# Optimization experiments

Hardware: AMD Instinct MI355X
Metric: run time of the kernel (lower is better)

Reference implementation:

```python
import jax, jax.numpy as jnp
import numpy as np

B, S, D = 16, 2048, 128

def setup_inputs() -> dict:
    key = jax.random.key(0)
    kq, kk, kv = jax.random.split(key, 3)
    queries = jax.random.normal(kq, (B, S, D), dtype=jnp.float32)
    keys = jax.random.normal(kk, (B, S, D), dtype=jnp.float32)
    values = jax.random.normal(kv, (B, S, D), dtype=jnp.float32)
    return {"queries": queries, "keys": keys, "values": values}

def reference(queries, keys, values):
    # scores: [B, S, S] = Q @ K^T / sqrt(D)
    d = queries.shape[-1]
    scores = jnp.einsum('bqd,bkd->bqk', queries, keys) / jnp.float32(np.sqrt(d))
    attn = jax.nn.softmax(scores, axis=-1)
    # dropout_rate=0.0 -> identity
    out = jnp.einsum('bqk,bkd->bqd', attn, values)
    return out
```

## Files before the change

kernel.cpp:

```cpp
#include <hip/hip_runtime.h>
#include <hip/hip_bf16.h>

#define BATCH 16
#define SEQ   2048
#define DIM   128
#define KTILE 64
#define NIT   (SEQ / KTILE)
#define NITP  (NIT / 2)
#define QT    128
#define SCALE2 (0.08838834764831845f * 1.4426950408889634f)

typedef __bf16 bf16_t;
typedef __bf16 bf16x8 __attribute__((ext_vector_type(8)));
typedef __bf16 bf16x4 __attribute__((ext_vector_type(4)));
typedef float  f32x4  __attribute__((ext_vector_type(4)));

#define KSTR 136

__device__ __forceinline__ int rho(int s) {
    return (s & 32) | ((s & 4) << 2) | (((s >> 3) & 3) << 2) | (s & 3);
}
__device__ __forceinline__ int swz(int row) {
    return (row & 7) ^ ((row >> 2) & 7);
}

__global__ __launch_bounds__(512, 2)
void attn_fwd(const float* __restrict__ Qg, const float* __restrict__ Kg,
              const float* __restrict__ Vg, float* __restrict__ Og)
{
    __shared__ __align__(16) bf16_t sK [4][KTILE][KSTR];
    __shared__ __align__(16) bf16_t sVt[4][DIM][64];

    const int tid  = threadIdx.x;
    const int wave = tid >> 6;
    const int lane = tid & 63;
    const int l16  = lane & 15;
    const int g    = lane >> 4;
    const bool is_comp = (wave < 4);

    const int bid   = blockIdx.x;
    const int batch = ((bid & 7) << 1) | ((bid >> 7) & 1);
    const int qtile = (bid >> 3) & 15;
    const int q0    = qtile * QT + wave * 32;

    const float* Kb = Kg + (size_t)batch * SEQ * DIM;
    const float* Vb = Vg + (size_t)batch * SEQ * DIM;

    bf16x8 qf[2][4];
    if (is_comp) {
        #pragma unroll
        for (int h = 0; h < 2; ++h) {
            const float* qp =
                Qg + ((size_t)batch * SEQ + q0 + h * 16 + l16) * DIM + g * 8;
            #pragma unroll
            for (int c = 0; c < 4; ++c) {
                const float4 u = *reinterpret_cast<const float4*>(qp + c * 32);
                const float4 v = *reinterpret_cast<const float4*>(qp + c * 32 + 4);
                bf16x8 f;
                f[0] = (bf16_t)(u.x * SCALE2); f[1] = (bf16_t)(u.y * SCALE2);
                f[2] = (bf16_t)(u.z * SCALE2); f[3] = (bf16_t)(u.w * SCALE2);
                f[4] = (bf16_t)(v.x * SCALE2); f[5] = (bf16_t)(v.y * SCALE2);
                f[6] = (bf16_t)(v.z * SCALE2); f[7] = (bf16_t)(v.w * SCALE2);
                qf[h][c] = f;
            }
        }
    }

    const int p    = tid & 255;
    const int krow = p >> 3;
    const int kch  = p & 7;
    const int vkg  = p >> 5;
    const int vd4  = p & 31;

    auto stage = [&](int k0, int buf) {
        float4 ka[2][2][2];
        float4 va[2][4];
        #pragma unroll
        for (int r = 0; r < 2; ++r)
            #pragma unroll
            for (int i = 0; i < 2; ++i) {
                const float* pp =
                    Kb + (size_t)(k0 + krow + r * 32) * DIM + kch * 8 + i * 64;
                ka[r][i][0] = *reinterpret_cast<const float4*>(pp);
                ka[r][i][1] = *reinterpret_cast<const float4*>(pp + 4);
            }
        #pragma unroll
        for (int r = 0; r < 2; ++r)
            #pragma unroll
            for (int j = 0; j < 4; ++j)
                va[r][j] = *reinterpret_cast<const float4*>(
                    Vb + (size_t)(k0 + (vkg + r * 8) * 4 + j) * DIM + vd4 * 4);
        #pragma unroll
        for (int r = 0; r < 2; ++r) {
            const int row = krow + r * 32;
            #pragma unroll
            for (int i = 0; i < 2; ++i) {
                const float* a = reinterpret_cast<const float*>(&ka[r][i][0]);
                bf16x8 w;
                #pragma unroll
                for (int e = 0; e < 8; ++e) w[e] = (bf16_t)a[e];
                *reinterpret_cast<bf16x8*>(&sK[buf][rho(row)][kch * 8 + i * 64]) = w;
            }
            const int kg = vkg + r * 8;
            #pragma unroll
            for (int dd = 0; dd < 4; ++dd) {
                const int vrow = vd4 * 4 + dd;
                const int col = (((kg >> 1) ^ swz(vrow)) << 3) + ((kg & 1) << 2);
                bf16x4 w;
                w[0] = (bf16_t)va[r][0][dd]; w[1] = (bf16_t)va[r][1][dd];
                w[2] = (bf16_t)va[r][2][dd]; w[3] = (bf16_t)va[r][3][dd];
                *reinterpret_cast<bf16x4*>(&sVt[buf][vrow][col]) = w;
            }
        }
    };

    const f32x4 vzero = {0.f, 0.f, 0.f, 0.f};
    f32x4 o[2][8];
    float lsum[2];
    if (is_comp) {
        #pragma unroll
        for (int h = 0; h < 2; ++h) {
            #pragma unroll
            for (int i = 0; i < 8; ++i) o[h][i] = vzero;
            lsum[h] = 0.f;
        }
    }

    if (!is_comp) {
        stage(0, 0);
        __builtin_amdgcn_sched_barrier(0);
        stage(KTILE, 1);
    }

    for (int t = 0; t < NITP; ++t) {
        __syncthreads();

        if (!is_comp) {
            if (t + 1 < NITP) {
                stage((2 * t + 2) * KTILE, (2 * t + 2) & 3);
                __builtin_amdgcn_sched_barrier(0);
                stage((2 * t + 3) * KTILE, (2 * t + 3) & 3);
            }
            continue;
        }

        #pragma unroll
        for (int s = 0; s < 2; ++s) {
            const int cur = (2 * t + s) & 3;

            f32x4 sc[2][4];
            #pragma unroll
            for (int ksb = 0; ksb < 4; ++ksb) { sc[0][ksb] = vzero; sc[1][ksb] = vzero; }
            __builtin_amdgcn_s_setprio(1);
            #pragma unroll
            for (int c = 0; c < 4; ++c) {
                #pragma unroll
                for (int ksb = 0; ksb < 4; ++ksb) {
                    bf16x8 kf = *reinterpret_cast<const bf16x8*>(
                        &sK[cur][ksb * 16 + l16][c * 32 + g * 8]);
                    sc[0][ksb] = __builtin_amdgcn_mfma_f32_16x16x32_bf16(
                        kf, qf[0][c], sc[0][ksb], 0, 0, 0);
                    sc[1][ksb] = __builtin_amdgcn_mfma_f32_16x16x32_bf16(
                        kf, qf[1][c], sc[1][ksb], 0, 0, 0);
                }
            }
            __builtin_amdgcn_s_setprio(0);

            float pe[2][16];
            #pragma unroll
            for (int h = 0; h < 2; ++h)
                #pragma unroll
                for (int ksb = 0; ksb < 4; ++ksb)
                    #pragma unroll
                    for (int r = 0; r < 4; ++r)
                        pe[h][ksb * 4 + r] = exp2f(sc[h][ksb][r]);
            #pragma unroll
            for (int h = 0; h < 2; ++h) {
                const float s0 = (pe[h][0] + pe[h][1]) + (pe[h][2] + pe[h][3]);
                const float s1 = (pe[h][4] + pe[h][5]) + (pe[h][6] + pe[h][7]);
                const float s2 = (pe[h][8] + pe[h][9]) + (pe[h][10] + pe[h][11]);
                const float s3 = (pe[h][12] + pe[h][13]) + (pe[h][14] + pe[h][15]);
                lsum[h] += (s0 + s1) + (s2 + s3);
            }
            bf16x8 pb[2][2];
            #pragma unroll
            for (int h = 0; h < 2; ++h)
                #pragma unroll
                for (int c2 = 0; c2 < 2; ++c2) {
                    bf16x8 tt;
                    #pragma unroll
                    for (int jj = 0; jj < 8; ++jj)
                        tt[jj] = (bf16_t)pe[h][(2 * c2 + (jj >> 2)) * 4 + (jj & 3)];
                    pb[h][c2] = tt;
                }

            __builtin_amdgcn_s_setprio(1);
            #pragma unroll
            for (int n0 = 0; n0 < 8; ++n0) {
                const int row = n0 * 16 + l16;
                #pragma unroll
                for (int c2 = 0; c2 < 2; ++c2) {
                    bf16x8 vf = *reinterpret_cast<const bf16x8*>(
                        &sVt[cur][row][((c2 * 4 + g) ^ swz(row)) << 3]);
                    o[0][n0] = __builtin_amdgcn_mfma_f32_16x16x32_bf16(
                        vf, pb[0][c2], o[0][n0], 0, 0, 0);
                    o[1][n0] = __builtin_amdgcn_mfma_f32_16x16x32_bf16(
                        vf, pb[1][c2], o[1][n0], 0, 0, 0);
                }
            }
            __builtin_amdgcn_s_setprio(0);
        }
    }

    if (is_comp) {
        #pragma unroll
        for (int h = 0; h < 2; ++h) {
            float l = lsum[h];
            l += __shfl_xor(l, 16);
            l += __shfl_xor(l, 32);
            const float inv = 1.f / l;
            float* op = Og + ((size_t)batch * SEQ + q0 + h * 16 + l16) * DIM + g * 4;
            #pragma unroll
            for (int n0 = 0; n0 < 8; ++n0) {
                float4 st = { o[h][n0][0] * inv, o[h][n0][1] * inv,
                              o[h][n0][2] * inv, o[h][n0][3] * inv };
                *reinterpret_cast<float4*>(op + n0 * 16) = st;
            }
        }
    }
}

extern "C" void kernel_launch(void* const* d_in, const int* in_sizes, int n_in,
                              void* d_out, int out_size, void* d_ws, size_t ws_size,
                              hipStream_t stream) {
    const float* Q = (const float*)d_in[0];
    const float* K = (const float*)d_in[1];
    const float* V = (const float*)d_in[2];
    float* O = (float*)d_out;
    dim3 grid(BATCH * SEQ / QT);
    dim3 block(512);
    hipLaunchKernelGGL(attn_fwd, grid, block, 0, stream, Q, K, V, O);
}
```

Before: 127.9 us.

## Split KV sequence across block pairs with cooperative grid sync to combine

```diff
diff --git a/kernel.cpp b/kernel.cpp
--- a/kernel.cpp
+++ b/kernel.cpp
@@ -1,13 +1,16 @@
 #include <hip/hip_runtime.h>
 #include <hip/hip_bf16.h>
+#include <hip/hip_cooperative_groups.h>
+
+namespace cg = cooperative_groups;
 
 #define BATCH 16
 #define SEQ   2048
 #define DIM   128
 #define KTILE 64
-#define NIT   (SEQ / KTILE)
-#define NITP  (NIT / 2)
-#define QT    128
+#define HALF  (SEQ / 2)
+#define NB    (HALF / KTILE)
+#define QT    256
 #define SCALE2 (0.08838834764831845f * 1.4426950408889634f)
 
 typedef __bf16 bf16_t;
@@ -26,204 +29,208 @@
 
 __global__ __launch_bounds__(512, 2)
 void attn_fwd(const float* __restrict__ Qg, const float* __restrict__ Kg,
-              const float* __restrict__ Vg, float* __restrict__ Og)
+              const float* __restrict__ Vg, float* __restrict__ Og,
+              float* __restrict__ lws)
 {
-    __shared__ __align__(16) bf16_t sK [4][KTILE][KSTR];
-    __shared__ __align__(16) bf16_t sVt[4][DIM][64];
+    __shared__ __align__(16) bf16_t sK [2][KTILE][KSTR];
+    __shared__ __align__(16) bf16_t sVt[2][DIM][64];
 
     const int tid  = threadIdx.x;
     const int wave = tid >> 6;
     const int lane = tid & 63;
     const int l16  = lane & 15;
     const int g    = lane >> 4;
-    const bool is_comp = (wave < 4);
 
     const int bid   = blockIdx.x;
-    const int batch = ((bid & 7) << 1) | ((bid >> 7) & 1);
-    const int qtile = (bid >> 3) & 15;
-    const int q0    = qtile * QT + wave * 32;
-
-    const float* Kb = Kg + (size_t)batch * SEQ * DIM;
-    const float* Vb = Vg + (size_t)batch * SEQ * DIM;
+    const int qt    = bid >> 1;
+    const int kv    = bid & 1;
+    const int batch = qt >> 3;
+    const int q0    = (qt & 7) * QT + wave * 32;
+
+    const float* Kb = Kg + ((size_t)batch * SEQ + kv * HALF) * DIM;
+    const float* Vb = Vg + ((size_t)batch * SEQ + kv * HALF) * DIM;
 
     bf16x8 qf[2][4];
-    if (is_comp) {
-        #pragma unroll
-        for (int h = 0; h < 2; ++h) {
-            const float* qp =
-                Qg + ((size_t)batch * SEQ + q0 + h * 16 + l16) * DIM + g * 8;
-            #pragma unroll
-            for (int c = 0; c < 4; ++c) {
-                const float4 u = *reinterpret_cast<const float4*>(qp + c * 32);
-                const float4 v = *reinterpret_cast<const float4*>(qp + c * 32 + 4);
-                bf16x8 f;
-                f[0] = (bf16_t)(u.x * SCALE2); f[1] = (bf16_t)(u.y * SCALE2);
-                f[2] = (bf16_t)(u.z * SCALE2); f[3] = (bf16_t)(u.w * SCALE2);
-                f[4] = (bf16_t)(v.x * SCALE2); f[5] = (bf16_t)(v.y * SCALE2);
-                f[6] = (bf16_t)(v.z * SCALE2); f[7] = (bf16_t)(v.w * SCALE2);
-                qf[h][c] = f;
-            }
-        }
-    }
-
-    const int p    = tid & 255;
-    const int krow = p >> 3;
-    const int kch  = p & 7;
-    const int vkg  = p >> 5;
-    const int vd4  = p & 31;
-
-    auto stage = [&](int k0, int buf) {
-        float4 ka[2][2][2];
-        float4 va[2][4];
-        #pragma unroll
-        for (int r = 0; r < 2; ++r)
-            #pragma unroll
-            for (int i = 0; i < 2; ++i) {
-                const float* pp =
-                    Kb + (size_t)(k0 + krow + r * 32) * DIM + kch * 8 + i * 64;
-                ka[r][i][0] = *reinterpret_cast<const float4*>(pp);
-                ka[r][i][1] = *reinterpret_cast<const float4*>(pp + 4);
-            }
-        #pragma unroll
-        for (int r = 0; r < 2; ++r)
-            #pragma unroll
-            for (int j = 0; j < 4; ++j)
-                va[r][j] = *reinterpret_cast<const float4*>(
-                    Vb + (size_t)(k0 + (vkg + r * 8) * 4 + j) * DIM + vd4 * 4);
-        #pragma unroll
-        for (int r = 0; r < 2; ++r) {
-            const int row = krow + r * 32;
-            #pragma unroll
-            for (int i = 0; i < 2; ++i) {
-                const float* a = reinterpret_cast<const float*>(&ka[r][i][0]);
-                bf16x8 w;
-                #pragma unroll
-                for (int e = 0; e < 8; ++e) w[e] = (bf16_t)a[e];
-                *reinterpret_cast<bf16x8*>(&sK[buf][rho(row)][kch * 8 + i * 64]) = w;
-            }
-            const int kg = vkg + r * 8;
-            #pragma unroll
-            for (int dd = 0; dd < 4; ++dd) {
-                const int vrow = vd4 * 4 + dd;
-                const int col = (((kg >> 1) ^ swz(vrow)) << 3) + ((kg & 1) << 2);
-                bf16x4 w;
-                w[0] = (bf16_t)va[r][0][dd]; w[1] = (bf16_t)va[r][1][dd];
-                w[2] = (bf16_t)va[r][2][dd]; w[3] = (bf16_t)va[r][3][dd];
-                *reinterpret_cast<bf16x4*>(&sVt[buf][vrow][col]) = w;
-            }
+    #pragma unroll
+    for (int h = 0; h < 2; ++h) {
+        const float* qp =
+            Qg + ((size_t)batch * SEQ + q0 + h * 16 + l16) * DIM + g * 8;
+        #pragma unroll
+        for (int c = 0; c < 4; ++c) {
+            const float4 u = *reinterpret_cast<const float4*>(qp + c * 32);
+            const float4 v = *reinterpret_cast<const float4*>(qp + c * 32 + 4);
+            bf16x8 f;
+            f[0] = (bf16_t)(u.x * SCALE2); f[1] = (bf16_t)(u.y * SCALE2);
+            f[2] = (bf16_t)(u.z * SCALE2); f[3] = (bf16_t)(u.w * SCALE2);
+            f[4] = (bf16_t)(v.x * SCALE2); f[5] = (bf16_t)(v.y * SCALE2);
+            f[6] = (bf16_t)(v.z * SCALE2); f[7] = (bf16_t)(v.w * SCALE2);
+            qf[h][c] = f;
+        }
+    }
+
+    const int krow = tid >> 3;
+    const int kch  = tid & 7;
+    const int vkg  = tid >> 5;
+    const int vd4  = tid & 31;
+
+    float4 gka[2][2];
+    float4 gva[4];
+
+    auto load_tile = [&](int k0) {
+        #pragma unroll
+        for (int i = 0; i < 2; ++i) {
+            const float* pp = Kb + (size_t)(k0 + krow) * DIM + kch * 8 + i * 64;
+            gka[i][0] = *reinterpret_cast<const float4*>(pp);
+            gka[i][1] = *reinterpret_cast<const float4*>(pp + 4);
+        }
+        #pragma unroll
+        for (int j = 0; j < 4; ++j)
+            gva[j] = *reinterpret_cast<const float4*>(
+                Vb + (size_t)(k0 + vkg * 4 + j) * DIM + vd4 * 4);
+    };
+    auto write_tile = [&](int buf) {
+        #pragma unroll
+        for (int i = 0; i < 2; ++i) {
+            const float* a = reinterpret_cast<const float*>(&gka[i][0]);
+            bf16x8 w;
+            #pragma unroll
+            for (int e = 0; e < 8; ++e) w[e] = (bf16_t)a[e];
+            *reinterpret_cast<bf16x8*>(&sK[buf][rho(krow)][kch * 8 + i * 64]) = w;
+        }
+        #pragma unroll
+        for (int dd = 0; dd < 4; ++dd) {
+            const int row = vd4 * 4 + dd;
+            const int col = (((vkg >> 1) ^ swz(row)) << 3) + ((vkg & 1) << 2);
+            bf16x4 w;
+            w[0] = (bf16_t)gva[0][dd]; w[1] = (bf16_t)gva[1][dd];
+            w[2] = (bf16_t)gva[2][dd]; w[3] = (bf16_t)gva[3][dd];
+            *reinterpret_cast<bf16x4*>(&sVt[buf][row][col]) = w;
         }
     };
 
     const f32x4 vzero = {0.f, 0.f, 0.f, 0.f};
     f32x4 o[2][8];
     float lsum[2];
-    if (is_comp) {
+    #pragma unroll
+    for (int h = 0; h < 2; ++h) {
+        #pragma unroll
+        for (int i = 0; i < 8; ++i) o[h][i] = vzero;
+        lsum[h] = 0.f;
+    }
+
+    load_tile(0);
+    write_tile(0);
+    load_tile(KTILE);
+    __syncthreads();
+
+    for (int t = 0; t < NB; ++t) {
+        const int cur = t & 1;
+
+        f32x4 sc[2][4];
+        #pragma unroll
+        for (int ksb = 0; ksb < 4; ++ksb) { sc[0][ksb] = vzero; sc[1][ksb] = vzero; }
+        __builtin_amdgcn_s_setprio(1);
+        #pragma unroll
+        for (int c = 0; c < 4; ++c) {
+            #pragma unroll
+            for (int ksb = 0; ksb < 4; ++ksb) {
+                bf16x8 kf = *reinterpret_cast<const bf16x8*>(
+                    &sK[cur][ksb * 16 + l16][c * 32 + g * 8]);
+                sc[0][ksb] = __builtin_amdgcn_mfma_f32_16x16x32_bf16(
+                    kf, qf[0][c], sc[0][ksb], 0, 0, 0);
+                sc[1][ksb] = __builtin_amdgcn_mfma_f32_16x16x32_bf16(
+                    kf, qf[1][c], sc[1][ksb], 0, 0, 0);
+            }
+        }
+        __builtin_amdgcn_s_setprio(0);
+
+        if (t + 1 < NB) write_tile(cur ^ 1);
+        if (t + 2 < NB) load_tile((t + 2) * KTILE);
+
+        float pe[2][16];
+        #pragma unroll
+        for (int h = 0; h < 2; ++h)
+            #pragma unroll
+            for (int ksb = 0; ksb < 4; ++ksb)
+                #pragma unroll
+                for (int r = 0; r < 4; ++r)
+                    pe[h][ksb * 4 + r] = exp2f(sc[h][ksb][r]);
         #pragma unroll
         for (int h = 0; h < 2; ++h) {
-            #pragma unroll
-            for (int i = 0; i < 8; ++i) o[h][i] = vzero;
-            lsum[h] = 0.f;
-        }
-    }
-
-    if (!is_comp) {
-        stage(0, 0);
-        __builtin_amdgcn_sched_barrier(0);
-        stage(KTILE, 1);
-    }
-
-    for (int t = 0; t < NITP; ++t) {
+            const float s0 = (pe[h][0] + pe[h][1]) + (pe[h][2] + pe[h][3]);
+            const float s1 = (pe[h][4] + pe[h][5]) + (pe[h][6] + pe[h][7]);
+            const float s2 = (pe[h][8] + pe[h][9]) + (pe[h][10] + pe[h][11]);
+            const float s3 = (pe[h][12] + pe[h][13]) + (pe[h][14] + pe[h][15]);
+            lsum[h] += (s0 + s1) + (s2 + s3);
+        }
+        bf16x8 pb[2][2];
+        #pragma unroll
+        for (int h = 0; h < 2; ++h)
+            #pragma unroll
+            for (int c2 = 0; c2 < 2; ++c2) {
+                bf16x8 tt;
+                #pragma unroll
+                for (int jj = 0; jj < 8; ++jj)
+                    tt[jj] = (bf16_t)pe[h][(2 * c2 + (jj >> 2)) * 4 + (jj & 3)];
+                pb[h][c2] = tt;
+            }
+
+        __builtin_amdgcn_s_setprio(1);
+        #pragma unroll
+        for (int n0 = 0; n0 < 8; ++n0) {
+            const int row = n0 * 16 + l16;
+            #pragma unroll
+            for (int c2 = 0; c2 < 2; ++c2) {
+                bf16x8 vf = *reinterpret_cast<const bf16x8*>(
+                    &sVt[cur][row][((c2 * 4 + g) ^ swz(row)) << 3]);
+                o[0][n0] = __builtin_amdgcn_mfma_f32_16x16x32_bf16(
+                    vf, pb[0][c2], o[0][n0], 0, 0, 0);
+                o[1][n0] = __builtin_amdgcn_mfma_f32_16x16x32_bf16(
+                    vf, pb[1][c2], o[1][n0], 0, 0, 0);
+            }
+        }
+        __builtin_amdgcn_s_setprio(0);
+
         __syncthreads();
-
-        if (!is_comp) {
-            if (t + 1 < NITP) {
-                stage((2 * t + 2) * KTILE, (2 * t + 2) & 3);
-                __builtin_amdgcn_sched_barrier(0);
-                stage((2 * t + 3) * KTILE, (2 * t + 3) & 3);
-            }
-            continue;
-        }
-
-        #pragma unroll
-        for (int s = 0; s < 2; ++s) {
-            const int cur = (2 * t + s) & 3;
-
-            f32x4 sc[2][4];
-            #pragma unroll
-            for (int ksb = 0; ksb < 4; ++ksb) { sc[0][ksb] = vzero; sc[1][ksb] = vzero; }
-            __builtin_amdgcn_s_setprio(1);
-            #pragma unroll
-            for (int c = 0; c < 4; ++c) {
-                #pragma unroll
-                for (int ksb = 0; ksb < 4; ++ksb) {
-                    bf16x8 kf = *reinterpret_cast<const bf16x8*>(
-                        &sK[cur][ksb * 16 + l16][c * 32 + g * 8]);
-                    sc[0][ksb] = __builtin_amdgcn_mfma_f32_16x16x32_bf16(
-                        kf, qf[0][c], sc[0][ksb], 0, 0, 0);
-                    sc[1][ksb] = __builtin_amdgcn_mfma_f32_16x16x32_bf16(
-                        kf, qf[1][c], sc[1][ksb], 0, 0, 0);
-                }
-            }
-            __builtin_amdgcn_s_setprio(0);
-
-            float pe[2][16];
-            #pragma unroll
-            for (int h = 0; h < 2; ++h)
-                #pragma unroll
-                for (int ksb = 0; ksb < 4; ++ksb)
-                    #pragma unroll
-                    for (int r = 0; r < 4; ++r)
-                        pe[h][ksb * 4 + r] = exp2f(sc[h][ksb][r]);
-            #pragma unroll
-            for (int h = 0; h < 2; ++h) {
-                const float s0 = (pe[h][0] + pe[h][1]) + (pe[h][2] + pe[h][3]);
-                const float s1 = (pe[h][4] + pe[h][5]) + (pe[h][6] + pe[h][7]);
-                const float s2 = (pe[h][8] + pe[h][9]) + (pe[h][10] + pe[h][11]);
-                const float s3 = (pe[h][12] + pe[h][13]) + (pe[h][14] + pe[h][15]);
-                lsum[h] += (s0 + s1) + (s2 + s3);
-            }
-            bf16x8 pb[2][2];
-            #pragma unroll
-            for (int h = 0; h < 2; ++h)
-                #pragma unroll
-                for (int c2 = 0; c2 < 2; ++c2) {
-                    bf16x8 tt;
-                    #pragma unroll
-                    for (int jj = 0; jj < 8; ++jj)
-                        tt[jj] = (bf16_t)pe[h][(2 * c2 + (jj >> 2)) * 4 + (jj & 3)];
-                    pb[h][c2] = tt;
-                }
-
-            __builtin_amdgcn_s_setprio(1);
+    }
+
+    float l[2];
+    #pragma unroll
+    for (int h = 0; h < 2; ++h) {
+        float v = lsum[h];
+        v += __shfl_xor(v, 16);
+        v += __shfl_xor(v, 32);
+        l[h] = v;
+    }
+
+    if (kv == 0) {
+        #pragma unroll
+        for (int h = 0; h < 2; ++h) {
+            float* op = Og + ((size_t)batch * SEQ + q0 + h * 16 + l16) * DIM + g * 4;
             #pragma unroll
             for (int n0 = 0; n0 < 8; ++n0) {
-                const int row = n0 * 16 + l16;
-                #pragma unroll
-                for (int c2 = 0; c2 < 2; ++c2) {
-                    bf16x8 vf = *reinterpret_cast<const bf16x8*>(
-                        &sVt[cur][row][((c2 * 4 + g) ^ swz(row)) << 3]);
-                    o[0][n0] = __builtin_amdgcn_mfma_f32_16x16x32_bf16(
-                        vf, pb[0][c2], o[0][n0], 0, 0, 0);
-                    o[1][n0] = __builtin_amdgcn_mfma_f32_16x16x32_bf16(
-                        vf, pb[1][c2], o[1][n0], 0, 0, 0);
-                }
-            }
-            __builtin_amdgcn_s_setprio(0);
-        }
-    }
-
-    if (is_comp) {
+                float4 st = { o[h][n0][0], o[h][n0][1], o[h][n0][2], o[h][n0][3] };
+                *reinterpret_cast<float4*>(op + n0 * 16) = st;
+            }
+            if (g == 0) lws[qt * QT + wave * 32 + h * 16 + l16] = l[h];
+        }
+    }
+    __threadfence();
+    cg::this_grid().sync();
+    __threadfence();
+    if (kv == 1) {
         #pragma unroll
         for (int h = 0; h < 2; ++h) {
-            float l = lsum[h];
-            l += __shfl_xor(l, 16);
-            l += __shfl_xor(l, 32);
-            const float inv = 1.f / l;
+            const float l0 = lws[qt * QT + wave * 32 + h * 16 + l16];
+            const float inv = 1.f / (l0 + l[h]);
             float* op = Og + ((size_t)batch * SEQ + q0 + h * 16 + l16) * DIM + g * 4;
             #pragma unroll
             for (int n0 = 0; n0 < 8; ++n0) {
-                float4 st = { o[h][n0][0] * inv, o[h][n0][1] * inv,
-                              o[h][n0][2] * inv, o[h][n0][3] * inv };
+                const float4 pr = *reinterpret_cast<const float4*>(op + n0 * 16);
+                float4 st = { (o[h][n0][0] + pr.x) * inv,
+                              (o[h][n0][1] + pr.y) * inv,
+                              (o[h][n0][2] + pr.z) * inv,
+                              (o[h][n0][3] + pr.w) * inv };
                 *reinterpret_cast<float4*>(op + n0 * 16) = st;
             }
         }
@@ -237,7 +244,9 @@
     const float* K = (const float*)d_in[1];
     const float* V = (const float*)d_in[2];
     float* O = (float*)d_out;
-    dim3 grid(BATCH * SEQ / QT);
+    float* lws = (float*)d_ws;
+    void* args[] = { (void*)&Q, (void*)&K, (void*)&V, (void*)&O, (void*)&lws };
+    dim3 grid(BATCH * SEQ / QT * 2);
     dim3 block(512);
-    hipLaunchKernelGGL(attn_fwd, grid, block, 0, stream, Q, K, V, O);
-}
+    hipLaunchCooperativeKernel((void*)attn_fwd, grid, block, args, 0, stream);
+}
```

New measurement: 278.6 us. +117.8%, slower.

## Split KV sequence across blocks with partial outputs and combine kernel

Applied to the files above, without the earlier changes.

```diff
diff --git a/kernel.cpp b/kernel.cpp
--- a/kernel.cpp
+++ b/kernel.cpp
@@ -5,9 +5,10 @@
 #define SEQ   2048
 #define DIM   128
 #define KTILE 64
-#define NIT   (SEQ / KTILE)
-#define NITP  (NIT / 2)
-#define QT    128
+#define HALF  (SEQ / 2)
+#define NB    (HALF / KTILE)
+#define QT    256
+#define NROW  (BATCH * SEQ)
 #define SCALE2 (0.08838834764831845f * 1.4426950408889634f)
 
 typedef __bf16 bf16_t;
@@ -25,8 +26,221 @@
 }
 
 __global__ __launch_bounds__(512, 2)
-void attn_fwd(const float* __restrict__ Qg, const float* __restrict__ Kg,
-              const float* __restrict__ Vg, float* __restrict__ Og)
+void attn_fwd_partial(const float* __restrict__ Qg, const float* __restrict__ Kg,
+                      const float* __restrict__ Vg, float* __restrict__ Og,
+                      float* __restrict__ lws)
+{
+    __shared__ __align__(16) bf16_t sK [2][KTILE][KSTR];
+    __shared__ __align__(16) bf16_t sVt[2][DIM][64];
+
+    const int tid  = threadIdx.x;
+    const int wave = tid >> 6;
+    const int lane = tid & 63;
+    const int l16  = lane & 15;
+    const int g    = lane >> 4;
+
+    const int bid  = blockIdx.x;
+    const int xcd  = bid & 7;
+    const int idx  = bid >> 3;
+    const int qtl  = idx & 7;
+    const int rest = idx >> 3;
+    const int sb   = rest & 1;
+    const int kv   = rest >> 1;
+    const int batch = (xcd << 1) | sb;
+    const int q0    = qtl * QT + wave * 32;
+
+    const float* Kb = Kg + ((size_t)batch * SEQ + kv * HALF) * DIM;
+    const float* Vb = Vg + ((size_t)batch * SEQ + kv * HALF) * DIM;
+
+    bf16x8 qf[2][4];
+    #pragma unroll
+    for (int h = 0; h < 2; ++h) {
+        const float* qp =
+            Qg + ((size_t)batch * SEQ + q0 + h * 16 + l16) * DIM + g * 8;
+        #pragma unroll
+        for (int c = 0; c < 4; ++c) {
+            const float4 u = *reinterpret_cast<const float4*>(qp + c * 32);
+            const float4 v = *reinterpret_cast<const float4*>(qp + c * 32 + 4);
+            bf16x8 f;
+            f[0] = (bf16_t)(u.x * SCALE2); f[1] = (bf16_t)(u.y * SCALE2);
+            f[2] = (bf16_t)(u.z * SCALE2); f[3] = (bf16_t)(u.w * SCALE2);
+            f[4] = (bf16_t)(v.x * SCALE2); f[5] = (bf16_t)(v.y * SCALE2);
+            f[6] = (bf16_t)(v.z * SCALE2); f[7] = (bf16_t)(v.w * SCALE2);
+            qf[h][c] = f;
+        }
+    }
+
+    const int krow = tid >> 3;
+    const int kch  = tid & 7;
+    const int vkg  = tid >> 5;
+    const int vd4  = tid & 31;
+
+    float4 gka[2][2];
+    float4 gva[4];
+
+    auto load_tile = [&](int k0) {
+        #pragma unroll
+        for (int i = 0; i < 2; ++i) {
+            const float* pp = Kb + (size_t)(k0 + krow) * DIM + kch * 8 + i * 64;
+            gka[i][0] = *reinterpret_cast<const float4*>(pp);
+            gka[i][1] = *reinterpret_cast<const float4*>(pp + 4);
+        }
+        #pragma unroll
+        for (int j = 0; j < 4; ++j)
+            gva[j] = *reinterpret_cast<const float4*>(
+                Vb + (size_t)(k0 + vkg * 4 + j) * DIM + vd4 * 4);
+    };
+    auto write_tile = [&](int buf) {
+        #pragma unroll
+        for (int i = 0; i < 2; ++i) {
+            const float* a = reinterpret_cast<const float*>(&gka[i][0]);
+            bf16x8 w;
+            #pragma unroll
+            for (int e = 0; e < 8; ++e) w[e] = (bf16_t)a[e];
+            *reinterpret_cast<bf16x8*>(&sK[buf][rho(krow)][kch * 8 + i * 64]) = w;
+        }
+        #pragma unroll
+        for (int dd = 0; dd < 4; ++dd) {
+            const int row = vd4 * 4 + dd;
+            const int col = (((vkg >> 1) ^ swz(row)) << 3) + ((vkg & 1) << 2);
+            bf16x4 w;
+            w[0] = (bf16_t)gva[0][dd]; w[1] = (bf16_t)gva[1][dd];
+            w[2] = (bf16_t)gva[2][dd]; w[3] = (bf16_t)gva[3][dd];
+            *reinterpret_cast<bf16x4*>(&sVt[buf][row][col]) = w;
+        }
+    };
+
+    const f32x4 vzero = {0.f, 0.f, 0.f, 0.f};
+    f32x4 o[2][8];
+    float lsum[2];
+    #pragma unroll
+    for (int h = 0; h < 2; ++h) {
+        #pragma unroll
+        for (int i = 0; i < 8; ++i) o[h][i] = vzero;
+        lsum[h] = 0.f;
+    }
+
+    load_tile(0);
+    write_tile(0);
+    load_tile(KTILE);
+    __syncthreads();
+
+    for (int t = 0; t < NB; ++t) {
+        const int cur = t & 1;
+
+        f32x4 sc[2][4];
+        #pragma unroll
+        for (int ksb = 0; ksb < 4; ++ksb) { sc[0][ksb] = vzero; sc[1][ksb] = vzero; }
+        __builtin_amdgcn_s_setprio(1);
+        #pragma unroll
+        for (int c = 0; c < 4; ++c) {
+            #pragma unroll
+            for (int ksb = 0; ksb < 4; ++ksb) {
+                bf16x8 kf = *reinterpret_cast<const bf16x8*>(
+                    &sK[cur][ksb * 16 + l16][c * 32 + g * 8]);
+                sc[0][ksb] = __builtin_amdgcn_mfma_f32_16x16x32_bf16(
+                    kf, qf[0][c], sc[0][ksb], 0, 0, 0);
+                sc[1][ksb] = __builtin_amdgcn_mfma_f32_16x16x32_bf16(
+                    kf, qf[1][c], sc[1][ksb], 0, 0, 0);
+            }
+        }
+        __builtin_amdgcn_s_setprio(0);
+
+        if (t + 1 < NB) write_tile(cur ^ 1);
+        if (t + 2 < NB) load_tile((t + 2) * KTILE);
+
+        float pe[2][16];
+        #pragma unroll
+        for (int h = 0; h < 2; ++h)
+            #pragma unroll
+            for (int ksb = 0; ksb < 4; ++ksb)
+                #pragma unroll
+                for (int r = 0; r < 4; ++r)
+                    pe[h][ksb * 4 + r] = exp2f(sc[h][ksb][r]);
+        #pragma unroll
+        for (int h = 0; h < 2; ++h) {
+            const float s0 = (pe[h][0] + pe[h][1]) + (pe[h][2] + pe[h][3]);
+            const float s1 = (pe[h][4] + pe[h][5]) + (pe[h][6] + pe[h][7]);
+            const float s2 = (pe[h][8] + pe[h][9]) + (pe[h][10] + pe[h][11]);
+            const float s3 = (pe[h][12] + pe[h][13]) + (pe[h][14] + pe[h][15]);
+            lsum[h] += (s0 + s1) + (s2 + s3);
+        }
+        bf16x8 pb[2][2];
+        #pragma unroll
+        for (int h = 0; h < 2; ++h)
+            #pragma unroll
+            for (int c2 = 0; c2 < 2; ++c2) {
+                bf16x8 tt;
+                #pragma unroll
+                for (int jj = 0; jj < 8; ++jj)
+                    tt[jj] = (bf16_t)pe[h][(2 * c2 + (jj >> 2)) * 4 + (jj & 3)];
+                pb[h][c2] = tt;
+            }
+
+        __builtin_amdgcn_s_setprio(1);
+        #pragma unroll
+        for (int n0 = 0; n0 < 8; ++n0) {
+            const int row = n0 * 16 + l16;
+            #pragma unroll
+            for (int c2 = 0; c2 < 2; ++c2) {
+                bf16x8 vf = *reinterpret_cast<const bf16x8*>(
+                    &sVt[cur][row][((c2 * 4 + g) ^ swz(row)) << 3]);
+                o[0][n0] = __builtin_amdgcn_mfma_f32_16x16x32_bf16(
+                    vf, pb[0][c2], o[0][n0], 0, 0, 0);
+                o[1][n0] = __builtin_amdgcn_mfma_f32_16x16x32_bf16(
+                    vf, pb[1][c2], o[1][n0], 0, 0, 0);
+            }
+        }
+        __builtin_amdgcn_s_setprio(0);
+
+        __syncthreads();
+    }
+
+    float l[2];
+    #pragma unroll
+    for (int h = 0; h < 2; ++h) {
+        float v = lsum[h];
+        v += __shfl_xor(v, 16);
+        v += __shfl_xor(v, 32);
+        l[h] = v;
+    }
+
+    float* Opart = (kv == 0) ? Og : (lws + 2 * NROW);
+    #pragma unroll
+    for (int h = 0; h < 2; ++h) {
+        const int row = batch * SEQ + q0 + h * 16 + l16;
+        float* op = Opart + (size_t)row * DIM + g * 4;
+        #pragma unroll
+        for (int n0 = 0; n0 < 8; ++n0) {
+            float4 st = { o[h][n0][0], o[h][n0][1], o[h][n0][2], o[h][n0][3] };
+            *reinterpret_cast<float4*>(op + n0 * 16) = st;
+        }
+        if (g == 0) lws[kv * NROW + row] = l[h];
+    }
+}
+
+__global__ __launch_bounds__(512)
+void attn_combine(float* __restrict__ Og, const float* __restrict__ lws)
+{
+    const int idx = blockIdx.x * 512 + threadIdx.x;
+    const int row = idx >> 5;
+    const float inv = 1.f / (lws[row] + lws[NROW + row]);
+    const float4* O1 = reinterpret_cast<const float4*>(lws + 2 * NROW);
+    float4* O0 = reinterpret_cast<float4*>(Og);
+    const float4 a = O0[idx];
+    const float4 b = O1[idx];
+    float4 st = { (a.x + b.x) * inv, (a.y + b.y) * inv,
+                  (a.z + b.z) * inv, (a.w + b.w) * inv };
+    O0[idx] = st;
+}
+
+#define NIT   (SEQ / KTILE)
+#define NITP  (NIT / 2)
+#define QTM   128
+
+__global__ __launch_bounds__(512, 2)
+void attn_fwd_mono(const float* __restrict__ Qg, const float* __restrict__ Kg,
+                   const float* __restrict__ Vg, float* __restrict__ Og)
 {
     __shared__ __align__(16) bf16_t sK [4][KTILE][KSTR];
     __shared__ __align__(16) bf16_t sVt[4][DIM][64];
@@ -41,7 +255,7 @@
     const int bid   = blockIdx.x;
     const int batch = ((bid & 7) << 1) | ((bid >> 7) & 1);
     const int qtile = (bid >> 3) & 15;
-    const int q0    = qtile * QT + wave * 32;
+    const int q0    = qtile * QTM + wave * 32;
 
     const float* Kb = Kg + (size_t)batch * SEQ * DIM;
     const float* Vb = Vg + (size_t)batch * SEQ * DIM;
@@ -147,7 +361,6 @@
         #pragma unroll
         for (int s = 0; s < 2; ++s) {
             const int cur = (2 * t + s) & 3;
-
             f32x4 sc[2][4];
             #pragma unroll
             for (int ksb = 0; ksb < 4; ++ksb) { sc[0][ksb] = vzero; sc[1][ksb] = vzero; }
@@ -237,7 +450,15 @@
     const float* K = (const float*)d_in[1];
     const float* V = (const float*)d_in[2];
     float* O = (float*)d_out;
-    dim3 grid(BATCH * SEQ / QT);
-    dim3 block(512);
-    hipLaunchKernelGGL(attn_fwd, grid, block, 0, stream, Q, K, V, O);
-}
+    const size_t WS_NEED = (size_t)(2 * NROW + (size_t)NROW * DIM) * sizeof(float);
+    if (ws_size >= WS_NEED) {
+        float* lws = (float*)d_ws;
+        hipLaunchKernelGGL(attn_fwd_partial, dim3(256), dim3(512), 0, stream,
+                           Q, K, V, O, lws);
+        hipLaunchKernelGGL(attn_combine, dim3(NROW * DIM / 4 / 512), dim3(512),
+                           0, stream, O, lws);
+    } else {
+        hipLaunchKernelGGL(attn_fwd_mono, dim3(BATCH * SEQ / QTM), dim3(512),
+                           0, stream, Q, K, V, O);
+    }
+}
```

Result: slower. 137.4 us (+7.4%).
